# Performance work log

Measured on AMD Instinct MI355X. Metric: run time of the kernel, lower is better.

The kernel has to match this reference:

```python
import jax, jax.numpy as jnp
import numpy as np

B, T, I, H = 64, 512, 64, 512
D1, D2, O = 1024, 2048, 16384


def setup_inputs() -> dict:
    key = jax.random.key(0)
    ks = jax.random.split(key, 16)
    bnd = 1.0 / np.sqrt(H)

    def u(k, shape):
        return jax.random.uniform(k, shape, minval=-bnd, maxval=bnd, dtype=jnp.float32)

    inp = {
        "x": jax.random.normal(ks[0], (B, T, I), dtype=jnp.float32),
        "Wih0": u(ks[1], (4 * H, I)),
        "Whh0": u(ks[2], (4 * H, H)),
        "bih0": u(ks[3], (4 * H,)).at[H:2 * H].set(1.0),
        "bhh0": u(ks[4], (4 * H,)).at[H:2 * H].set(1.0),
        "Wih1": u(ks[5], (4 * H, H)),
        "Whh1": u(ks[6], (4 * H, H)),
        "bih1": u(ks[7], (4 * H,)).at[H:2 * H].set(1.0),
        "bhh1": u(ks[8], (4 * H,)).at[H:2 * H].set(1.0),
        "W1": jax.random.normal(ks[9], (D1, H), dtype=jnp.float32) * 0.05,
        "b1": jnp.zeros((D1,), jnp.float32),
        "W2": jax.random.normal(ks[10], (D2, D1), dtype=jnp.float32) * 0.03,
        "b2": jnp.zeros((D2,), jnp.float32),
        "W3": jax.random.normal(ks[11], (O, D2), dtype=jnp.float32) * 0.02,
        "b3": jnp.zeros((O,), jnp.float32),
    }
    return inp


def _cell(x_t, h, c, Wih, Whh, bih, bhh):
    # x_t: [B, in], h/c: [B, H]; gates: [B, 4H]
    gates = x_t @ Wih.T + h @ Whh.T + (bih + bhh)
    i, f, g, o = jnp.split(gates, 4, axis=-1)
    i = jax.nn.sigmoid(i)
    f = jax.nn.sigmoid(f)
    g = jnp.tanh(g)
    o = jax.nn.sigmoid(o)
    c_new = f * c + i * g
    h_new = o * jnp.tanh(c_new)
    return h_new, c_new


def reference(x, Wih0, Whh0, bih0, bhh0, Wih1, Whh1, bih1, bhh1,
              W1, b1, W2, b2, W3, b3):
    Bn = x.shape[0]
    z = jnp.zeros((Bn, H), x.dtype)
    xT = jnp.swapaxes(x, 0, 1)  # [T, B, I]

    def step(carry, x_t):
        h0, c0, h1, c1 = carry
        h0, c0 = _cell(x_t, h0, c0, Wih0, Whh0, bih0, bhh0)
        h1, c1 = _cell(h0, h1, c1, Wih1, Whh1, bih1, bhh1)
        return (h0, c0, h1, c1), None

    (h0, c0, h1, c1), _ = jax.lax.scan(step, (z, z, z, z), xT)
    # decoder MLP on final top-layer hidden state (== outputs[-1])
    y = jax.nn.relu(h1 @ W1.T + b1)
    y = jax.nn.relu(y @ W2.T + b2)
    return y @ W3.T + b3  # [B, O]
```

## Files before the change

kernel.cpp:

```cpp
#include <hip/hip_runtime.h>
#include <hip/hip_bf16.h>
#include <cstdio>


#define B_  64
#define T_  512
#define I_  64
#define H_  512
#define D1_ 1024
#define D2_ 2048
#define O_  16384

typedef __attribute__((ext_vector_type(8))) short bf16x8_t;
typedef __attribute__((ext_vector_type(4))) float f32x4_t;
typedef unsigned short ushort_t;

__device__ inline ushort_t f2bf(float f) {
    return __builtin_bit_cast(ushort_t, __float2bfloat16(f));
}
__device__ inline float sigm(float x) { return 1.0f / (1.0f + __expf(-x)); }
__device__ inline float tanhf_(float x) {
    float cx = fminf(fmaxf(x, -15.f), 15.f);
    float e = __expf(2.f * cx);
    return (e - 1.f) / (e + 1.f);
}


__global__ void pack_l0(const float* __restrict__ Wih0, const float* __restrict__ Whh0,
                        ushort_t* __restrict__ pack) {
    int idx = blockIdx.x * 256 + threadIdx.x;
    int l  = idx & 63;
    int kk = (idx >> 6) % 18;
    int tu = idx / (18 * 64);
    int jl = l & 15, g8 = (l >> 4) * 8;
    int gate = jl & 3, u = tu * 4 + (jl >> 2);
    int wrow = gate * H_ + u;
    int kg = kk * 32 + g8;
    const float* s = (kg < H_) ? (Whh0 + (size_t)wrow * H_ + kg)
                               : (Wih0 + (size_t)wrow * I_ + (kg - H_));
    ushort_t* d = pack + (size_t)idx * 8;
#pragma unroll
    for (int i = 0; i < 8; i++) d[i] = f2bf(s[i]);
}

__global__ void pack_l1(const float* __restrict__ Wih1, const float* __restrict__ Whh1,
                        ushort_t* __restrict__ pack) {
    int idx = blockIdx.x * 256 + threadIdx.x;
    int l  = idx & 63;
    int kk = (idx >> 6) & 31;
    int tu = idx >> 11;
    int jl = l & 15, g8 = (l >> 4) * 8;
    int gate = jl & 3, u = tu * 4 + (jl >> 2);
    int wrow = gate * H_ + u;
    int kg = kk * 32 + g8;
    const float* s = (kg < H_) ? (Wih1 + (size_t)wrow * H_ + kg)
                               : (Whh1 + (size_t)wrow * H_ + (kg - H_));
    ushort_t* d = pack + (size_t)idx * 8;
#pragma unroll
    for (int i = 0; i < 8; i++) d[i] = f2bf(s[i]);
}

__global__ void pack_bias(const float* __restrict__ bih0, const float* __restrict__ bhh0,
                          const float* __restrict__ bih1, const float* __restrict__ bhh1,
                          float* __restrict__ bsum) {
    int idx = blockIdx.x * 256 + threadIdx.x;
    int layer = idx >> 11;
    int rest = idx & 2047;
    int u = rest >> 2, gate = rest & 3;
    const float* a = layer ? bih1 : bih0;
    const float* b = layer ? bhh1 : bhh0;
    bsum[idx] = a[gate * H_ + u] + b[gate * H_ + u];
}

__global__ void conv_x(const float* __restrict__ x, ushort_t* __restrict__ xbf) {
    int idx = blockIdx.x * 256 + threadIdx.x;
    int c = idx & 63;
    int t = (idx >> 6) & 511;
    int b = idx >> 15;
    xbf[(size_t)t * 4096 + b * 64 + c] = f2bf(x[idx]);
}


__device__ inline void grid_barrier(unsigned int* flags, int iter, int tid, int wg) {
    asm volatile("s_waitcnt vmcnt(0)" ::: "memory");
    __syncthreads();
    unsigned int target = (unsigned int)(iter + 1);
    if (tid == 0)
        __hip_atomic_store(&flags[wg], target, __ATOMIC_RELAXED,
                           __HIP_MEMORY_SCOPE_AGENT);
    if (tid < 64) {
        const uint4* fp = (const uint4*)flags;
        for (;;) {
            uint4 f;
            asm volatile("global_load_dwordx4 %0, %1, off sc0 sc1"
                         : "=v"(f) : "v"(fp + tid));
            asm volatile("s_waitcnt vmcnt(0)" ::: "memory");
            bool ok = (f.x >= target) & (f.y >= target) &
                      (f.z >= target) & (f.w >= target);
            if (__all(ok)) break;
            __builtin_amdgcn_s_sleep(2);
        }
    }
    __syncthreads();
}

template <int LAYER>
__device__ void run_layer(int tu, int tid, int wg,
                          const ushort_t* __restrict__ pack,
                          const float* __restrict__ bsum,
                          const ushort_t* __restrict__ xbf,
                          ushort_t* __restrict__ hbuf0,
                          ushort_t* __restrict__ hbuf1,
                          unsigned int* __restrict__ flags)
{
    constexpr int NK = LAYER ? 32 : 18;
    int l = tid & 63, v = tid >> 6;
    int u_loc = l >> 4;
    int bb = v * 16 + (l & 15);
    int u = tu * 4 + u_loc;
    int g8 = u_loc * 8;

    bf16x8_t aF[NK];
    {
        const ushort_t* src = pack + (size_t)tu * (NK * 512) + l * 8;
#pragma unroll
        for (int kk = 0; kk < NK; ++kk)
            aF[kk] = *(const bf16x8_t*)(src + kk * 512);
    }
    const float* bp = bsum + LAYER * 2048 + u * 4;
    float bi0 = bp[0], bi1 = bp[1], bi2 = bp[2], bi3 = bp[3];
    float creg = 0.0f;

    const int HS = 64 * 512;
    for (int k = 0; k <= T_; ++k) {
        bool active = LAYER ? (k >= 1) : (k < T_);
        if (active) {
            const ushort_t* h0r = hbuf0 + ((k + 1) & 1) * HS + bb * 512;
            const ushort_t* srcHi = LAYER ? (hbuf1 + (k & 1) * HS + bb * 512)
                                          : (xbf + (size_t)k * 4096 + bb * 64);
            bf16x8_t bfr[NK];
#pragma unroll
            for (int kk = 0; kk < NK; ++kk) {
                if (!LAYER && kk >= 16) {
                    bfr[kk] = *(const bf16x8_t*)(srcHi + (kk - 16) * 32 + g8);
                } else {
                    const ushort_t* q = (kk < 16) ? (h0r + kk * 32 + g8)
                                                  : (srcHi + (kk - 16) * 32 + g8);
                    asm volatile("global_load_dwordx4 %0, %1, off sc0 sc1"
                                 : "=v"(bfr[kk]) : "v"(q));
                }
            }
            asm volatile("s_waitcnt vmcnt(0)" ::: "memory");
            __builtin_amdgcn_sched_barrier(0);
            f32x4_t acc  = {bi0, bi1, bi2, bi3};
            f32x4_t acc2 = {0.f, 0.f, 0.f, 0.f};
#pragma unroll
            for (int kk = 0; kk < NK; ++kk) {
                if (kk & 1)
                    acc2 = __builtin_amdgcn_mfma_f32_16x16x32_bf16(aF[kk], bfr[kk], acc2, 0, 0, 0);
                else
                    acc  = __builtin_amdgcn_mfma_f32_16x16x32_bf16(aF[kk], bfr[kk], acc, 0, 0, 0);
            }
            acc = acc + acc2;
            float xi = sigm(acc[0]);
            float xf = sigm(acc[1]);
            float xg = tanhf_(acc[2]);
            float xo = sigm(acc[3]);
            creg = xf * creg + xi * xg;
            float hn = xo * tanhf_(creg);
            ushort_t* hw = LAYER ? (hbuf1 + ((k + 1) & 1) * HS)
                                 : (hbuf0 + (k & 1) * HS);
            unsigned int mine = (unsigned int)f2bf(hn);
            unsigned int other = (unsigned int)__shfl_xor((int)mine, 16, 64);
            if ((u_loc & 1) == 0) {
                unsigned int valp = mine | (other << 16);
                __hip_atomic_store((unsigned int*)(hw + (size_t)bb * 512 + u), valp,
                                   __ATOMIC_RELAXED, __HIP_MEMORY_SCOPE_AGENT);
            }
        }
        if (k < T_)
            grid_barrier(flags, k, tid, wg);
    }
}

__global__ __launch_bounds__(256, 1) void lstm_persist(
    const ushort_t* __restrict__ packL0, const ushort_t* __restrict__ packL1,
    const float* __restrict__ bsum, const ushort_t* __restrict__ xbf,
    ushort_t* __restrict__ hbuf0, ushort_t* __restrict__ hbuf1,
    unsigned int* __restrict__ flags)
{
    int w = blockIdx.x, tid = threadIdx.x;
    if (w < 128)
        run_layer<0>(w, tid, w, packL0, bsum, xbf, hbuf0, hbuf1, flags);
    else
        run_layer<1>(w - 128, tid, w, packL1, bsum, xbf, hbuf0, hbuf1, flags);
}

template <int NK, bool RELU, bool OUTBF>
__global__ __launch_bounds__(256) void dec_gemm(
    const float* __restrict__ W, const float* __restrict__ bias,
    const ushort_t* __restrict__ act, void* __restrict__ outp, int ncols)
{
    int tile = blockIdx.x, tid = threadIdx.x;
    int l = tid & 63, v = tid >> 6;
    int bb = v * 16 + (l & 15);
    int jA = tile * 16 + (l & 15);
    int g8 = (l >> 4) * 8;
    const float* wrow = W + (size_t)jA * (NK * 32);
    const ushort_t* arow = act + (size_t)bb * (NK * 32);
    f32x4_t acc = {0.f, 0.f, 0.f, 0.f};
    for (int kk = 0; kk < NK; ++kk) {
        int kg = kk * 32 + g8;
        float4 w0 = *(const float4*)(wrow + kg);
        float4 w1 = *(const float4*)(wrow + kg + 4);
        bf16x8_t af;
        af[0] = (short)f2bf(w0.x); af[1] = (short)f2bf(w0.y);
        af[2] = (short)f2bf(w0.z); af[3] = (short)f2bf(w0.w);
        af[4] = (short)f2bf(w1.x); af[5] = (short)f2bf(w1.y);
        af[6] = (short)f2bf(w1.z); af[7] = (short)f2bf(w1.w);
        bf16x8_t bf = *(const bf16x8_t*)(arow + kg);
        acc = __builtin_amdgcn_mfma_f32_16x16x32_bf16(af, bf, acc, 0, 0, 0);
    }
    int j0 = tile * 16 + (l >> 4) * 4;
    float r[4];
#pragma unroll
    for (int i = 0; i < 4; i++) {
        r[i] = acc[i] + bias[j0 + i];
        if (RELU) r[i] = fmaxf(r[i], 0.f);
    }
    if (OUTBF) {
        ushort_t* o = (ushort_t*)outp + (size_t)bb * ncols + j0;
        unsigned int lo = (unsigned)f2bf(r[0]) | ((unsigned)f2bf(r[1]) << 16);
        unsigned int hi = (unsigned)f2bf(r[2]) | ((unsigned)f2bf(r[3]) << 16);
        uint2 q; q.x = lo; q.y = hi;
        *(uint2*)o = q;
    } else {
        float* o = (float*)outp + (size_t)bb * ncols + j0;
        float4 t4; t4.x = r[0]; t4.y = r[1]; t4.z = r[2]; t4.w = r[3];
        *(float4*)o = t4;
    }
}

extern "C" void kernel_launch(void* const* d_in, const int* in_sizes, int n_in,
                              void* d_out, int out_size, void* d_ws, size_t ws_size,
                              hipStream_t stream)
{
    const float* x    = (const float*)d_in[0];
    const float* Wih0 = (const float*)d_in[1];
    const float* Whh0 = (const float*)d_in[2];
    const float* bih0 = (const float*)d_in[3];
    const float* bhh0 = (const float*)d_in[4];
    const float* Wih1 = (const float*)d_in[5];
    const float* Whh1 = (const float*)d_in[6];
    const float* bih1 = (const float*)d_in[7];
    const float* bhh1 = (const float*)d_in[8];
    const float* W1   = (const float*)d_in[9];
    const float* b1   = (const float*)d_in[10];
    const float* W2   = (const float*)d_in[11];
    const float* b2   = (const float*)d_in[12];
    const float* W3   = (const float*)d_in[13];
    const float* b3   = (const float*)d_in[14];

    char* ws = (char*)d_ws;
    size_t off = 0;
    auto take = [&](size_t bytes) -> char* {
        char* p = ws + off;
        off = (off + bytes + 255) & ~(size_t)255;
        return p;
    };
    ushort_t* packL0 = (ushort_t*)take((size_t)128 * 18 * 64 * 8 * 2);
    ushort_t* packL1 = (ushort_t*)take((size_t)128 * 32 * 64 * 8 * 2);
    float*    bsum   = (float*)take(2 * 2048 * 4);
    ushort_t* xbf    = (ushort_t*)take((size_t)512 * 64 * 64 * 2);
    char* zbase = ws + off;
    ushort_t* hbuf0  = (ushort_t*)take(2 * 64 * 512 * 2);
    ushort_t* hbuf1  = (ushort_t*)take(2 * 64 * 512 * 2);
    unsigned int* flags = (unsigned int*)take(256 * 4);
    size_t zbytes = (size_t)((ws + off) - zbase);
    ushort_t* y1 = (ushort_t*)take(64 * 1024 * 2);
    ushort_t* y2 = (ushort_t*)take(64 * 2048 * 2);
    if (off > ws_size) {
        fprintf(stderr, "kernel_launch: ws too small: need %zu have %zu\n", off, ws_size);
        return;
    }

    pack_l0<<<(128 * 18 * 64) / 256, 256, 0, stream>>>(Wih0, Whh0, packL0);
    pack_l1<<<(128 * 32 * 64) / 256, 256, 0, stream>>>(Wih1, Whh1, packL1);
    pack_bias<<<16, 256, 0, stream>>>(bih0, bhh0, bih1, bhh1, bsum);
    conv_x<<<(64 * 512 * 64) / 256, 256, 0, stream>>>(x, xbf);
    hipMemsetAsync(zbase, 0, zbytes, stream);

    lstm_persist<<<256, 256, 0, stream>>>(packL0, packL1, bsum, xbf,
                                          hbuf0, hbuf1, flags);

    const ushort_t* h1f = hbuf1 + 1 * (64 * 512);
    dec_gemm<16, true,  true ><<<  64, 256, 0, stream>>>(W1, b1, h1f, y1, D1_);
    dec_gemm<32, true,  true ><<< 128, 256, 0, stream>>>(W2, b2, y1, y2, D2_);
    dec_gemm<64, false, false><<<1024, 256, 0, stream>>>(W3, b3, y2, d_out, O_);
}
```

Measured before the change: 5.429 ms.

## Shrink persistent LSTM grid to 64 workgroups, four unit tiles each

The persistent LSTM kernel now runs on 64 workgroups instead of 256, and each workgroup handles four unit-tiles, so the per-step grid barrier polls 64 flags with a single dword load per lane. This is meant to cut the cost of the 512 grid-wide barriers. In exchange, weights are no longer held in registers. They are reloaded from global memory (L2) on every timestep, and each workgroup does four times more MFMA and activation work per step, which lengthens the critical path.

Result: slower. 9.998 ms (+84.2%).

```diff
diff --git a/kernel.cpp b/kernel.cpp
--- a/kernel.cpp
+++ b/kernel.cpp
@@ -81,6 +81,8 @@
 }
 
 
+#define NWG 64
+
 __device__ inline void grid_barrier(unsigned int* flags, int iter, int tid, int wg) {
     asm volatile("s_waitcnt vmcnt(0)" ::: "memory");
     __syncthreads();
@@ -89,15 +91,12 @@
         __hip_atomic_store(&flags[wg], target, __ATOMIC_RELAXED,
                            __HIP_MEMORY_SCOPE_AGENT);
     if (tid < 64) {
-        const uint4* fp = (const uint4*)flags;
         for (;;) {
-            uint4 f;
-            asm volatile("global_load_dwordx4 %0, %1, off sc0 sc1"
-                         : "=v"(f) : "v"(fp + tid));
+            unsigned int f;
+            asm volatile("global_load_dword %0, %1, off sc0 sc1"
+                         : "=v"(f) : "v"(flags + tid));
             asm volatile("s_waitcnt vmcnt(0)" ::: "memory");
-            bool ok = (f.x >= target) & (f.y >= target) &
-                      (f.z >= target) & (f.w >= target);
-            if (__all(ok)) break;
+            if (__all(f >= target)) break;
             __builtin_amdgcn_s_sleep(2);
         }
     }
@@ -105,7 +104,7 @@
 }
 
 template <int LAYER>
-__device__ void run_layer(int tu, int tid, int wg,
+__device__ void run_layer(int wg, int tid,
                           const ushort_t* __restrict__ pack,
                           const float* __restrict__ bsum,
                           const ushort_t* __restrict__ xbf,
@@ -114,22 +113,24 @@
                           unsigned int* __restrict__ flags)
 {
     constexpr int NK = LAYER ? 32 : 18;
+    constexpr int UG = 4;
     int l = tid & 63, v = tid >> 6;
     int u_loc = l >> 4;
     int bb = v * 16 + (l & 15);
-    int u = tu * 4 + u_loc;
     int g8 = u_loc * 8;
-
-    bf16x8_t aF[NK];
-    {
-        const ushort_t* src = pack + (size_t)tu * (NK * 512) + l * 8;
-#pragma unroll
-        for (int kk = 0; kk < NK; ++kk)
-            aF[kk] = *(const bf16x8_t*)(src + kk * 512);
-    }
-    const float* bp = bsum + LAYER * 2048 + u * 4;
-    float bi0 = bp[0], bi1 = bp[1], bi2 = bp[2], bi3 = bp[3];
-    float creg = 0.0f;
+    int tu0 = (LAYER ? (wg - 32) : wg) * UG;
+
+    const ushort_t* wbase[UG];
+    float bi[UG][4];
+    float creg[UG];
+#pragma unroll
+    for (int t = 0; t < UG; ++t) {
+        wbase[t] = pack + (size_t)(tu0 + t) * (NK * 512) + l * 8;
+        int u = (tu0 + t) * 4 + u_loc;
+        const float* bp = bsum + LAYER * 2048 + u * 4;
+        bi[t][0] = bp[0]; bi[t][1] = bp[1]; bi[t][2] = bp[2]; bi[t][3] = bp[3];
+        creg[t] = 0.0f;
+    }
 
     const int HS = 64 * 512;
     for (int k = 0; k <= T_; ++k) {
@@ -152,30 +153,38 @@
             }
             asm volatile("s_waitcnt vmcnt(0)" ::: "memory");
             __builtin_amdgcn_sched_barrier(0);
-            f32x4_t acc  = {bi0, bi1, bi2, bi3};
-            f32x4_t acc2 = {0.f, 0.f, 0.f, 0.f};
+            f32x4_t acc[UG];
+#pragma unroll
+            for (int t = 0; t < UG; ++t) {
+                acc[t][0] = bi[t][0]; acc[t][1] = bi[t][1];
+                acc[t][2] = bi[t][2]; acc[t][3] = bi[t][3];
+            }
 #pragma unroll
             for (int kk = 0; kk < NK; ++kk) {
-                if (kk & 1)
-                    acc2 = __builtin_amdgcn_mfma_f32_16x16x32_bf16(aF[kk], bfr[kk], acc2, 0, 0, 0);
-                else
-                    acc  = __builtin_amdgcn_mfma_f32_16x16x32_bf16(aF[kk], bfr[kk], acc, 0, 0, 0);
+#pragma unroll
+                for (int t = 0; t < UG; ++t) {
+                    bf16x8_t a = *(const bf16x8_t*)(wbase[t] + kk * 512);
+                    acc[t] = __builtin_amdgcn_mfma_f32_16x16x32_bf16(a, bfr[kk], acc[t], 0, 0, 0);
+                }
             }
-            acc = acc + acc2;
-            float xi = sigm(acc[0]);
-            float xf = sigm(acc[1]);
-            float xg = tanhf_(acc[2]);
-            float xo = sigm(acc[3]);
-            creg = xf * creg + xi * xg;
-            float hn = xo * tanhf_(creg);
             ushort_t* hw = LAYER ? (hbuf1 + ((k + 1) & 1) * HS)
                                  : (hbuf0 + (k & 1) * HS);
-            unsigned int mine = (unsigned int)f2bf(hn);
-            unsigned int other = (unsigned int)__shfl_xor((int)mine, 16, 64);
-            if ((u_loc & 1) == 0) {
-                unsigned int valp = mine | (other << 16);
-                __hip_atomic_store((unsigned int*)(hw + (size_t)bb * 512 + u), valp,
-                                   __ATOMIC_RELAXED, __HIP_MEMORY_SCOPE_AGENT);
+#pragma unroll
+            for (int t = 0; t < UG; ++t) {
+                float xi = sigm(acc[t][0]);
+                float xf = sigm(acc[t][1]);
+                float xg = tanhf_(acc[t][2]);
+                float xo = sigm(acc[t][3]);
+                creg[t] = xf * creg[t] + xi * xg;
+                float hn = xo * tanhf_(creg[t]);
+                unsigned int mine = (unsigned int)f2bf(hn);
+                unsigned int other = (unsigned int)__shfl_xor((int)mine, 16, 64);
+                if ((u_loc & 1) == 0) {
+                    int u = (tu0 + t) * 4 + u_loc;
+                    unsigned int valp = mine | (other << 16);
+                    __hip_atomic_store((unsigned int*)(hw + (size_t)bb * 512 + u), valp,
+                                       __ATOMIC_RELAXED, __HIP_MEMORY_SCOPE_AGENT);
+                }
             }
         }
         if (k < T_)
@@ -190,10 +199,10 @@
     unsigned int* __restrict__ flags)
 {
     int w = blockIdx.x, tid = threadIdx.x;
-    if (w < 128)
-        run_layer<0>(w, tid, w, packL0, bsum, xbf, hbuf0, hbuf1, flags);
+    if (w < 32)
+        run_layer<0>(w, tid, packL0, bsum, xbf, hbuf0, hbuf1, flags);
     else
-        run_layer<1>(w - 128, tid, w, packL1, bsum, xbf, hbuf0, hbuf1, flags);
+        run_layer<1>(w, tid, packL1, bsum, xbf, hbuf0, hbuf1, flags);
 }
 
 template <int NK, bool RELU, bool OUTBF>
@@ -275,7 +284,7 @@
     char* zbase = ws + off;
     ushort_t* hbuf0  = (ushort_t*)take(2 * 64 * 512 * 2);
     ushort_t* hbuf1  = (ushort_t*)take(2 * 64 * 512 * 2);
-    unsigned int* flags = (unsigned int*)take(256 * 4);
+    unsigned int* flags = (unsigned int*)take(NWG * 4);
     size_t zbytes = (size_t)((ws + off) - zbase);
     ushort_t* y1 = (ushort_t*)take(64 * 1024 * 2);
     ushort_t* y2 = (ushort_t*)take(64 * 2048 * 2);
@@ -290,7 +299,7 @@
     conv_x<<<(64 * 512 * 64) / 256, 256, 0, stream>>>(x, xbf);
     hipMemsetAsync(zbase, 0, zbytes, stream);
 
-    lstm_persist<<<256, 256, 0, stream>>>(packL0, packL1, bsum, xbf,
+    lstm_persist<<<NWG, 256, 0, stream>>>(packL0, packL1, bsum, xbf,
                                           hbuf0, hbuf1, flags);
 
     const ushort_t* h1f = hbuf1 + 1 * (64 * 512);
```
